# Optimization experiments

Hardware: AMD Instinct MI355X
Metric: run time of the kernel (lower is better)

The kernel has to match this reference:

```python
import jax, jax.numpy as jnp
import numpy as np


def _flip_neg(a):
    # index k -> a[(-k) mod n] along last axis (torch.roll(torch.flip(a,-1),1,-1))
    return jnp.roll(jnp.flip(a, axis=-1), 1, axis=-1)


def setup_inputs() -> dict:
    key = jax.random.key(0)
    k1, k2 = jax.random.split(key)
    B, C, L, M = 16, 64, 65536, 512
    x = jax.random.normal(k1, (B, C, L), dtype=jnp.float32)
    scale = 1.0 / (C * C)
    weights1 = scale * jax.random.uniform(k2, (C, C, M), dtype=jnp.float32)
    return {"x": x, "weights1": weights1}


def reference(x, weights1):
    B, Cin, L = x.shape
    M = weights1.shape[-1]
    two_pi = jnp.asarray(2.0 * np.pi, dtype=x.dtype)

    # pseudo-DHT: elementwise modulation along length
    k = jnp.arange(L, dtype=x.dtype)
    theta = two_pi * k / L
    x_ht = x * (jnp.cos(theta) - jnp.sin(theta))  # (B, Cin, L)

    # mode-limited channel mixing (compl_mul1d)
    x1 = x_ht[:, :, :M]                 # (B, Cin, M)
    x1n = _flip_neg(x1)
    wn = _flip_neg(weights1)
    out_m = 0.5 * (
        jnp.einsum('bix,iox->box', x1, weights1)
        - jnp.einsum('bix,iox->box', x1n, wn)
        + jnp.einsum('bix,iox->box', x1, wn)
        + jnp.einsum('bix,iox->box', x1n, weights1)
    )  # (B, Cout, M)

    # zero-init half-spectrum buffer, slice-assign low modes
    Lh = L // 2 + 1
    Cout = weights1.shape[1]
    out = jnp.zeros((B, Cout, Lh), dtype=x.dtype).at[:, :, :M].set(out_m)

    # idht: same pseudo-DHT on the (B, Cout, Lh) buffer, normalized by size(1)=channels
    k2 = jnp.arange(Lh, dtype=x.dtype)
    theta2 = two_pi * k2 / Lh
    out = out * (jnp.cos(theta2) - jnp.sin(theta2)) / Cin
    return out
```

## Files before the change

### kernel.cpp

```cpp
#include <hip/hip_runtime.h>
#include <math.h>

#define B_   16
#define CIN  64
#define COUT 64
#define L_   65536
#define M_   512
#define LH_  32769

#define NBLK     2048
#define NTHREADS (NBLK * 256)
#define N4       ((B_ * COUT * LH_) / 4)

__global__ __launch_bounds__(256) void fused_spectral(
    const float* __restrict__ x, const float* __restrict__ w, float* __restrict__ out)
{
    const int tid = blockIdx.x * 256 + threadIdx.x;

    for (int j = tid; j < N4; j += NTHREADS) {
        const unsigned flat = (unsigned)j * 4u;
        const unsigned row  = flat / (unsigned)LH_;
        const unsigned col  = flat - row * (unsigned)LH_;
        if (col >= (unsigned)M_ && col <= (unsigned)(LH_ - 4)) {
            const float4 z = {0.f, 0.f, 0.f, 0.f};
            reinterpret_cast<float4*>(out)[j] = z;
        } else {
            #pragma unroll
            for (int e = 0; e < 4; ++e) {
                const unsigned f  = flat + (unsigned)e;
                const unsigned r2 = f / (unsigned)LH_;
                const unsigned c2_ = f - r2 * (unsigned)LH_;
                if (c2_ >= (unsigned)M_) out[f] = 0.f;
            }
        }
    }

    if (threadIdx.x >= 64) return;
    const int ctid = blockIdx.x * 64 + (int)threadIdx.x;
    const int m  = ctid & (M_ - 1);
    const int og = (ctid >> 9) & 15;
    const int b  = ctid >> 13;
    const int o0 = og * 4;
    const int m2 = (M_ - m) & (M_ - 1);

    const float TWO_PI = 6.28318530717958647692f;
    const float t1  = TWO_PI * (float)m  / (float)L_;
    const float t1n = TWO_PI * (float)m2 / (float)L_;
    const float t2  = TWO_PI * (float)m  / (float)LH_;
    const float c1m = cosf(t1)  - sinf(t1);
    const float c1n = cosf(t1n) - sinf(t1n);
    const float c2  = (cosf(t2) - sinf(t2)) * (1.0f / (float)CIN);

    float acc[4] = {0.f, 0.f, 0.f, 0.f};
    const float* xb = x + (size_t)b * CIN * L_;
    for (int i = 0; i < CIN; ++i) {
        const float xm = xb[(size_t)i * L_ + m]  * c1m;
        const float xn = xb[(size_t)i * L_ + m2] * c1n;
        const float* wr = w + ((size_t)i * COUT + o0) * M_;
        #pragma unroll
        for (int oo = 0; oo < 4; ++oo) {
            const float wm = wr[(size_t)oo * M_ + m];
            const float wn = wr[(size_t)oo * M_ + m2];
            acc[oo] += xm * (wm + wn) + xn * (wm - wn);
        }
    }

    #pragma unroll
    for (int oo = 0; oo < 4; ++oo)
        out[(size_t)(b * COUT + o0 + oo) * LH_ + m] = 0.5f * c2 * acc[oo];
}

extern "C" void kernel_launch(void* const* d_in, const int* in_sizes, int n_in,
                              void* d_out, int out_size, void* d_ws, size_t ws_size,
                              hipStream_t stream) {
    const float* x = (const float*)d_in[0];
    const float* w = (const float*)d_in[1];
    float* out = (float*)d_out;

    fused_spectral<<<NBLK, 256, 0, stream>>>(x, w, out);
}
```

Before: 38.55 us.

## Tile channel-mix as 2 batches x 2 outputs and use nontemporal zero stores

Zero-fill stores now use nontemporal builtins so the large output memset bypasses cache retention. The mode-mixing phase changes each thread's work from 4 output channels for one batch to a 2x2 tile of batches and output channels. Each weight load is now reused across two batches and each x load across two outputs. The inner loop is unrolled and the 0.5 factor is folded into c2. The cost is more x loads per output and a different block-to-work mapping.

```diff
diff --git a/kernel.cpp b/kernel.cpp
--- a/kernel.cpp
+++ b/kernel.cpp
@@ -12,35 +12,37 @@
 #define NTHREADS (NBLK * 256)
 #define N4       ((B_ * COUT * LH_) / 4)
 
+typedef float f4 __attribute__((ext_vector_type(4)));
+
 __global__ __launch_bounds__(256) void fused_spectral(
     const float* __restrict__ x, const float* __restrict__ w, float* __restrict__ out)
 {
-    const int tid = blockIdx.x * 256 + threadIdx.x;
+    const int tid = (int)blockIdx.x * 256 + (int)threadIdx.x;
 
     for (int j = tid; j < N4; j += NTHREADS) {
         const unsigned flat = (unsigned)j * 4u;
         const unsigned row  = flat / (unsigned)LH_;
         const unsigned col  = flat - row * (unsigned)LH_;
         if (col >= (unsigned)M_ && col <= (unsigned)(LH_ - 4)) {
-            const float4 z = {0.f, 0.f, 0.f, 0.f};
-            reinterpret_cast<float4*>(out)[j] = z;
+            const f4 z = {0.f, 0.f, 0.f, 0.f};
+            __builtin_nontemporal_store(z, reinterpret_cast<f4*>(out) + j);
         } else {
             #pragma unroll
             for (int e = 0; e < 4; ++e) {
                 const unsigned f  = flat + (unsigned)e;
                 const unsigned r2 = f / (unsigned)LH_;
                 const unsigned c2_ = f - r2 * (unsigned)LH_;
-                if (c2_ >= (unsigned)M_) out[f] = 0.f;
+                if (c2_ >= (unsigned)M_) __builtin_nontemporal_store(0.f, out + f);
             }
         }
     }
 
     if (threadIdx.x >= 64) return;
-    const int ctid = blockIdx.x * 64 + (int)threadIdx.x;
-    const int m  = ctid & (M_ - 1);
-    const int og = (ctid >> 9) & 15;
-    const int b  = ctid >> 13;
-    const int o0 = og * 4;
+    const int cw   = (int)blockIdx.x;
+    const int lane = (int)threadIdx.x;
+    const int m  = ((cw & 7) << 6) + lane;
+    const int o0 = ((cw >> 3) & 31) * 2;
+    const int b0 = (cw >> 8) * 2;
     const int m2 = (M_ - m) & (M_ - 1);
 
     const float TWO_PI = 6.28318530717958647692f;
@@ -49,25 +51,37 @@
     const float t2  = TWO_PI * (float)m  / (float)LH_;
     const float c1m = cosf(t1)  - sinf(t1);
     const float c1n = cosf(t1n) - sinf(t1n);
-    const float c2  = (cosf(t2) - sinf(t2)) * (1.0f / (float)CIN);
+    const float c2  = (cosf(t2) - sinf(t2)) * (0.5f / (float)CIN);
 
-    float acc[4] = {0.f, 0.f, 0.f, 0.f};
-    const float* xb = x + (size_t)b * CIN * L_;
+    float a00 = 0.f, a01 = 0.f, a10 = 0.f, a11 = 0.f;
+
+    const float* xA = x + (size_t)b0 * CIN * L_;
+    const float* xB = xA + (size_t)CIN * L_;
+
+    #pragma unroll 4
     for (int i = 0; i < CIN; ++i) {
-        const float xm = xb[(size_t)i * L_ + m]  * c1m;
-        const float xn = xb[(size_t)i * L_ + m2] * c1n;
-        const float* wr = w + ((size_t)i * COUT + o0) * M_;
-        #pragma unroll
-        for (int oo = 0; oo < 4; ++oo) {
-            const float wm = wr[(size_t)oo * M_ + m];
-            const float wn = wr[(size_t)oo * M_ + m2];
-            acc[oo] += xm * (wm + wn) + xn * (wm - wn);
-        }
+        const size_t ro = (size_t)i * L_;
+        const float xmA = xA[ro + m]  * c1m;
+        const float xnA = xA[ro + m2] * c1n;
+        const float xmB = xB[ro + m]  * c1m;
+        const float xnB = xB[ro + m2] * c1n;
+
+        const float* wr = w + (size_t)(i * COUT + o0) * M_;
+        const float wm0 = wr[m],      wn0 = wr[m2];
+        const float wm1 = wr[M_ + m], wn1 = wr[M_ + m2];
+        const float ws0 = wm0 + wn0, wd0 = wm0 - wn0;
+        const float ws1 = wm1 + wn1, wd1 = wm1 - wn1;
+
+        a00 += xmA * ws0 + xnA * wd0;
+        a01 += xmA * ws1 + xnA * wd1;
+        a10 += xmB * ws0 + xnB * wd0;
+        a11 += xmB * ws1 + xnB * wd1;
     }
 
-    #pragma unroll
-    for (int oo = 0; oo < 4; ++oo)
-        out[(size_t)(b * COUT + o0 + oo) * LH_ + m] = 0.5f * c2 * acc[oo];
+    out[(size_t)((b0 + 0) * COUT + o0 + 0) * LH_ + m] = c2 * a00;
+    out[(size_t)((b0 + 0) * COUT + o0 + 1) * LH_ + m] = c2 * a01;
+    out[(size_t)((b0 + 1) * COUT + o0 + 0) * LH_ + m] = c2 * a10;
+    out[(size_t)((b0 + 1) * COUT + o0 + 1) * LH_ + m] = c2 * a11;
 }
 
 extern "C" void kernel_launch(void* const* d_in, const int* in_sizes, int n_in,
```

Result: slower. 69.23 us (+79.6%).
